# Optimization experiments

Hardware: AMD Instinct MI355X
Metric: run time of the kernel (lower is better)

The kernel has to match this reference:

```python
import jax, jax.numpy as jnp
import numpy as np

B, S, D = 2, 4096, 768
H = 12
HD = D // H  # 64
SCALE = HD ** -0.5


def setup_inputs() -> dict:
    key = jax.random.key(0)
    ks = jax.random.split(key, 5)
    return {
        "x": jax.random.normal(ks[0], (B, S, D), dtype=jnp.float32),
        "qkv_w": jax.random.normal(ks[1], (D, 3 * D), dtype=jnp.float32) * (D ** -0.5),
        "qkv_b": jax.random.normal(ks[2], (3 * D,), dtype=jnp.float32) * 0.02,
        "proj_w": jax.random.normal(ks[3], (D, D), dtype=jnp.float32) * (D ** -0.5),
        "proj_b": jax.random.normal(ks[4], (D,), dtype=jnp.float32) * 0.02,
    }


def reference(x, qkv_w, qkv_b, proj_w, proj_b):
    b, s, d = x.shape
    qkv = x @ qkv_w + qkv_b                      # [B, S, 3D]
    qkv = qkv.reshape(b, s, 3, H, HD)
    q, k, v = jnp.moveaxis(qkv, 2, 0)            # each [B, S, H, HD]
    q = jnp.swapaxes(q, 1, 2)                    # [B, H, S, HD]
    k = jnp.swapaxes(k, 1, 2)
    v = jnp.swapaxes(v, 1, 2)
    attn = jnp.einsum("bhqd,bhkd->bhqk", q, k) * SCALE  # [B, H, S, S]
    attn = jax.nn.softmax(attn, axis=-1)
    out = jnp.einsum("bhqk,bhkd->bhqd", attn, v)        # [B, H, S, HD]
    out = jnp.swapaxes(out, 1, 2).reshape(b, s, d)      # [B, S, D]
    return out @ proj_w + proj_b
```

## Files before the change

### kernel.cpp

```cpp
#include <hip/hip_runtime.h>

typedef unsigned short u16;
typedef __attribute__((ext_vector_type(8))) short bf16x8;
typedef __attribute__((ext_vector_type(4))) float f32x4;
typedef __attribute__((ext_vector_type(16))) float f32x16;

__device__ __forceinline__ u16 f2bf(float f) {
  union { float f; unsigned u; } v; v.f = f;
  unsigned r = v.u + 0x7fffu + ((v.u >> 16) & 1u);
  return (u16)(r >> 16);
}
__device__ __forceinline__ float bf2f(u16 h) {
  union { unsigned u; float f; } v; v.u = ((unsigned)h) << 16;
  return v.f;
}

__device__ __forceinline__ bf16x8 ld_frag(const char* p) {
  union { uint4 u; bf16x8 v; } t;
  t.u = *(const uint4*)p;
  return t.v;
}

__global__ __launch_bounds__(256) void k_prep(const float* __restrict__ x,
                                              const float* __restrict__ qkv_w,
                                              const float* __restrict__ proj_w,
                                              u16* __restrict__ xb,
                                              u16* __restrict__ wt,
                                              u16* __restrict__ pwt) {
  int bid = blockIdx.x, tid = threadIdx.x;
  if (bid < 6144) {
    int i = bid * 256 + tid;
    float4 v = ((const float4*)x)[i];
    ushort4 o; o.x = f2bf(v.x); o.y = f2bf(v.y); o.z = f2bf(v.z); o.w = f2bf(v.w);
    ((ushort4*)xb)[i] = o;
    return;
  }
  __shared__ float tile[32][33];
  const float* in; u16* out; int R, C, bx, by;
  if (bid < 6144 + 1728) {
    int t = bid - 6144; in = qkv_w; out = wt; R = 768; C = 2304;
    bx = (t % 72) * 32; by = (t / 72) * 32;
  } else {
    int t = bid - 7872; in = proj_w; out = pwt; R = 768; C = 768;
    bx = (t % 24) * 32; by = (t / 24) * 32;
  }
  int tx = tid & 31, ty = tid >> 5;
#pragma unroll
  for (int j = 0; j < 32; j += 8)
    tile[ty + j][tx] = in[(size_t)(by + ty + j) * C + bx + tx];
  __syncthreads();
#pragma unroll
  for (int j = 0; j < 32; j += 8)
    out[(size_t)(bx + ty + j) * R + by + tx] = f2bf(tile[tx][ty + j]);
}

#define GAS(p) ((const __attribute__((address_space(1))) void*)(p))
#define LAS(p) ((__attribute__((address_space(3))) void*)(p))

__global__ __launch_bounds__(256) void k_gemm_qkv(
    const u16* __restrict__ A,
    const u16* __restrict__ Bt,
    const float* __restrict__ bias,
    u16* __restrict__ Qb, u16* __restrict__ Kb, u16* __restrict__ Vb) {
  const int K = 768;
  __shared__ u16 Al[128 * 64];
  __shared__ u16 Bl[128 * 64];
  int tn0 = blockIdx.x * 128, tm0 = blockIdx.y * 128;
  int tid = threadIdx.x, w = tid >> 6, lane = tid & 63;
  int l16 = lane & 15, lg = lane >> 4;
  int wm = (w >> 1) * 64, wn = (w & 1) * 64;
  f32x4 acc[4][4];
#pragma unroll
  for (int fm = 0; fm < 4; ++fm)
#pragma unroll
    for (int fn = 0; fn < 4; ++fn) acc[fm][fn] = (f32x4){0.f, 0.f, 0.f, 0.f};
  int srow = w * 32 + (lane >> 3);
  int scol = (lane & 7) * 8;
  for (int k0 = 0; k0 < K; k0 += 64) {
#pragma unroll
    for (int i = 0; i < 4; ++i) {
      __builtin_amdgcn_global_load_lds(GAS(A + (size_t)(tm0 + srow + i * 8) * K + k0 + scol),
                                       LAS((char*)Al + w * 4096 + i * 1024 + lane * 16), 16, 0, 0);
      __builtin_amdgcn_global_load_lds(GAS(Bt + (size_t)(tn0 + srow + i * 8) * K + k0 + scol),
                                       LAS((char*)Bl + w * 4096 + i * 1024 + lane * 16), 16, 0, 0);
    }
    __syncthreads();
#pragma unroll
    for (int ks = 0; ks < 2; ++ks) {
      bf16x8 af[4], bv[4];
#pragma unroll
      for (int f = 0; f < 4; ++f)
        af[f] = *(const bf16x8*)&Al[(wm + f * 16 + l16) * 64 + lg * 8 + ks * 32];
#pragma unroll
      for (int f = 0; f < 4; ++f)
        bv[f] = *(const bf16x8*)&Bl[(wn + f * 16 + l16) * 64 + lg * 8 + ks * 32];
#pragma unroll
      for (int fm = 0; fm < 4; ++fm)
#pragma unroll
        for (int fn = 0; fn < 4; ++fn)
          acc[fm][fn] = __builtin_amdgcn_mfma_f32_16x16x32_bf16(af[fm], bv[fn], acc[fm][fn], 0, 0, 0);
    }
    __syncthreads();
  }
  int part = tn0 / 768;
  u16* dst = part == 0 ? Qb : (part == 1 ? Kb : Vb);
  float qscale = (part == 0) ? 0.18033688011112042f : 1.0f;
#pragma unroll
  for (int fn = 0; fn < 4; ++fn) {
    int nn = tn0 + wn + fn * 16 + l16;
    float bvs = bias[nn];
    int np = nn - part * 768;
    int hh = np >> 6, hd = np & 63;
#pragma unroll
    for (int fm = 0; fm < 4; ++fm) {
#pragma unroll
      for (int r = 0; r < 4; ++r) {
        int m = tm0 + wm + fm * 16 + lg * 4 + r;
        int bb = m >> 12, s = m & 4095;
        size_t idx;
        if (part == 2) {
          int sp = (s & ~12) | ((s & 8) >> 1) | ((s & 4) << 1);
          idx = (((size_t)(bb * 12 + hh)) * 64 + hd) * 4096 + sp;
        } else {
          idx = (((size_t)(bb * 12 + hh)) * 4096 + s) * 64 + hd;
        }
        dst[idx] = f2bf((acc[fm][fn][r] + bvs) * qscale);
      }
    }
  }
}

__global__ __launch_bounds__(256) void k_gemm_proj(
    const u16* __restrict__ A,
    const u16* __restrict__ Bt,
    const float* __restrict__ bias, float* __restrict__ out) {
  const int K = 768;
  __shared__ u16 Al[128 * 64];
  __shared__ u16 Bl[128 * 64];
  int tn0 = blockIdx.x * 128, tm0 = blockIdx.y * 128;
  int tid = threadIdx.x, w = tid >> 6, lane = tid & 63;
  int l16 = lane & 15, lg = lane >> 4;
  int wm = (w >> 1) * 64, wn = (w & 1) * 64;
  f32x4 acc[4][4];
#pragma unroll
  for (int fm = 0; fm < 4; ++fm)
#pragma unroll
    for (int fn = 0; fn < 4; ++fn) acc[fm][fn] = (f32x4){0.f, 0.f, 0.f, 0.f};
  int srow = w * 32 + (lane >> 3);
  int scol = (lane & 7) * 8;
  for (int k0 = 0; k0 < K; k0 += 64) {
#pragma unroll
    for (int i = 0; i < 4; ++i) {
      __builtin_amdgcn_global_load_lds(GAS(A + (size_t)(tm0 + srow + i * 8) * K + k0 + scol),
                                       LAS((char*)Al + w * 4096 + i * 1024 + lane * 16), 16, 0, 0);
      __builtin_amdgcn_global_load_lds(GAS(Bt + (size_t)(tn0 + srow + i * 8) * K + k0 + scol),
                                       LAS((char*)Bl + w * 4096 + i * 1024 + lane * 16), 16, 0, 0);
    }
    __syncthreads();
#pragma unroll
    for (int ks = 0; ks < 2; ++ks) {
      bf16x8 af[4], bv[4];
#pragma unroll
      for (int f = 0; f < 4; ++f)
        af[f] = *(const bf16x8*)&Al[(wm + f * 16 + l16) * 64 + lg * 8 + ks * 32];
#pragma unroll
      for (int f = 0; f < 4; ++f)
        bv[f] = *(const bf16x8*)&Bl[(wn + f * 16 + l16) * 64 + lg * 8 + ks * 32];
#pragma unroll
      for (int fm = 0; fm < 4; ++fm)
#pragma unroll
        for (int fn = 0; fn < 4; ++fn)
          acc[fm][fn] = __builtin_amdgcn_mfma_f32_16x16x32_bf16(af[fm], bv[fn], acc[fm][fn], 0, 0, 0);
    }
    __syncthreads();
  }
#pragma unroll
  for (int fn = 0; fn < 4; ++fn) {
    int nn = tn0 + wn + fn * 16 + l16;
    float bvs = bias[nn];
#pragma unroll
    for (int fm = 0; fm < 4; ++fm) {
#pragma unroll
      for (int r = 0; r < 4; ++r) {
        int m = tm0 + wm + fm * 16 + lg * 4 + r;
        out[(size_t)m * 768 + nn] = acc[fm][fn][r] + bvs;
      }
    }
  }
}

__global__ __launch_bounds__(256, 3) void k_attn(const u16* __restrict__ Qb,
                                                 const u16* __restrict__ Kb,
                                                 const u16* __restrict__ Vtg,
                                                 u16* __restrict__ Ob) {
  const int S = 4096, NH = 12, D = 768;
  __shared__ u16 Kl[2][64 * 64];
  __shared__ u16 Vl[2][64 * 64];

  int bid0 = blockIdx.x;
  int bid = (bid0 & 7) * 96 + (bid0 >> 3);
  int qp = bid & 31;
  int bh = bid >> 5;
  int b = bh / NH, h = bh % NH;
  const u16* Qh = Qb + (size_t)bh * S * 64;
  const char* Khc = (const char*)(Kb + (size_t)bh * S * 64);
  const char* Vhc = (const char*)(Vtg + (size_t)bh * 64 * S);

  int tid = threadIdx.x, w = tid >> 6, lane = tid & 63;
  int q31 = lane & 31, hi = lane >> 5;
  int swb = (q31 & 7) << 4;
  int coff = (hi << 4);

  unsigned xoff[4];
#pragma unroll
  for (int ks = 0; ks < 4; ++ks)
    xoff[ks] = (unsigned)(q31 * 128 + ((ks * 32 + coff) ^ swb));

  int r8 = lane >> 3;
  int chs = (lane & 7) ^ r8;
  const char* kSrc = Khc + (size_t)(w * 16 + r8) * 128 + chs * 16;
  const char* vSrc = Vhc + (size_t)(w * 16 + r8) * 8192 + chs * 16;
  char* kDst0 = (char*)&Kl[0][0] + w * 2048 + lane * 16;
  char* vDst0 = (char*)&Vl[0][0] + w * 2048 + lane * 16;

  auto STAGE = [&](int bufi, int kv) {
#pragma unroll
    for (int qq = 0; qq < 2; ++qq) {
      __builtin_amdgcn_global_load_lds(GAS(kSrc + (size_t)kv * 8192 + qq * 1024),
                                       LAS(kDst0 + bufi * 8192 + qq * 1024), 16, 0, 0);
      __builtin_amdgcn_global_load_lds(GAS(vSrc + (size_t)qq * 65536 + (size_t)kv * 128),
                                       LAS(vDst0 + bufi * 8192 + qq * 1024), 16, 0, 0);
    }
  };

  int qbase = qp * 128 + w * 32;
  const u16* qrow = Qh + (size_t)(qbase + q31) * 64;
  bf16x8 qf[4];
#pragma unroll
  for (int ks = 0; ks < 4; ++ks)
    qf[ks] = *(const bf16x8*)(qrow + ks * 16 + hi * 8);

  f32x16 of0, of1, la0, la1;
#pragma unroll
  for (int i = 0; i < 16; ++i) { of0[i] = 0.f; of1[i] = 0.f; la0[i] = 0.f; la1[i] = 0.f; }

  auto TILE = [&](const char* KB, const char* VB) {
    f32x16 s0, s1;
#pragma unroll
    for (int i = 0; i < 16; ++i) { s0[i] = 0.f; s1[i] = 0.f; }
    __builtin_amdgcn_s_setprio(1);
#pragma unroll
    for (int ks = 0; ks < 4; ++ks) {
      bf16x8 kf = ld_frag(KB + xoff[ks]);
      s0 = __builtin_amdgcn_mfma_f32_32x32x16_bf16(kf, qf[ks], s0, 0, 0, 0);
    }
#pragma unroll
    for (int ks = 0; ks < 4; ++ks) {
      bf16x8 kf = ld_frag(KB + 4096 + xoff[ks]);
      s1 = __builtin_amdgcn_mfma_f32_32x32x16_bf16(kf, qf[ks], s1, 0, 0, 0);
    }
    __builtin_amdgcn_s_setprio(0);
#pragma unroll
    for (int i = 0; i < 16; ++i) {
      s0[i] = __builtin_amdgcn_exp2f(s0[i]);
      s1[i] = __builtin_amdgcn_exp2f(s1[i]);
    }
    la0 += s0;
    la1 += s1;
    union U8 { unsigned u[4]; bf16x8 v; };
    bf16x8 pf[4];
#define MK_PF(DST, SS, R0)                                                        \
    { U8 tt;                                                                      \
      asm("v_cvt_pk_bf16_f32 %0,%1,%2" : "=v"(tt.u[0]) : "v"(SS[R0+0]), "v"(SS[R0+1])); \
      asm("v_cvt_pk_bf16_f32 %0,%1,%2" : "=v"(tt.u[1]) : "v"(SS[R0+2]), "v"(SS[R0+3])); \
      asm("v_cvt_pk_bf16_f32 %0,%1,%2" : "=v"(tt.u[2]) : "v"(SS[R0+4]), "v"(SS[R0+5])); \
      asm("v_cvt_pk_bf16_f32 %0,%1,%2" : "=v"(tt.u[3]) : "v"(SS[R0+6]), "v"(SS[R0+7])); \
      DST = tt.v; }
    MK_PF(pf[0], s0, 0); MK_PF(pf[1], s0, 8);
    MK_PF(pf[2], s1, 0); MK_PF(pf[3], s1, 8);
#undef MK_PF
    __builtin_amdgcn_s_setprio(1);
#pragma unroll
    for (int ks = 0; ks < 4; ++ks) {
      bf16x8 vf = ld_frag(VB + xoff[ks]);
      of0 = __builtin_amdgcn_mfma_f32_32x32x16_bf16(vf, pf[ks], of0, 0, 0, 0);
    }
#pragma unroll
    for (int ks = 0; ks < 4; ++ks) {
      bf16x8 vf = ld_frag(VB + 4096 + xoff[ks]);
      of1 = __builtin_amdgcn_mfma_f32_32x32x16_bf16(vf, pf[ks], of1, 0, 0, 0);
    }
    __builtin_amdgcn_s_setprio(0);
  };

  const char* K0 = (const char*)&Kl[0][0];
  const char* K1 = (const char*)&Kl[1][0];
  const char* V0 = (const char*)&Vl[0][0];
  const char* V1 = (const char*)&Vl[1][0];

  STAGE(0, 0);
  __syncthreads();

#pragma unroll 1
  for (int kv = 0; kv < S / 64; kv += 2) {
    STAGE(1, kv + 1);
    TILE(K0, V0);
    __syncthreads();
    if (kv + 2 < S / 64) STAGE(0, kv + 2);
    TILE(K1, V1);
    if (kv + 2 < S / 64) __syncthreads();
  }

  float ts[8];
#pragma unroll
  for (int i = 0; i < 8; ++i) ts[i] = (la0[i] + la0[i + 8]) + (la1[i] + la1[i + 8]);
#pragma unroll
  for (int st = 4; st >= 1; st >>= 1)
#pragma unroll
    for (int i = 0; i < 4; ++i)
      if (i < st) ts[i] += ts[i + st];
  float l_full = ts[0] + __shfl_xor(ts[0], 32, 64);
  float inv = 1.f / l_full;
  int q = qbase + q31;
  u16* orow = Ob + (size_t)(b * S + q) * D + h * 64;
#pragma unroll
  for (int g = 0; g < 4; ++g) {
    ushort4 o0, o1;
    o0.x = f2bf(of0[g * 4 + 0] * inv); o0.y = f2bf(of0[g * 4 + 1] * inv);
    o0.z = f2bf(of0[g * 4 + 2] * inv); o0.w = f2bf(of0[g * 4 + 3] * inv);
    o1.x = f2bf(of1[g * 4 + 0] * inv); o1.y = f2bf(of1[g * 4 + 1] * inv);
    o1.z = f2bf(of1[g * 4 + 2] * inv); o1.w = f2bf(of1[g * 4 + 3] * inv);
    int hd0 = g * 8 + hi * 4;
    *(ushort4*)(orow + hd0) = o0;
    *(ushort4*)(orow + 32 + hd0) = o1;
  }
}

extern "C" void kernel_launch(void* const* d_in, const int* in_sizes, int n_in,
                              void* d_out, int out_size, void* d_ws, size_t ws_size,
                              hipStream_t stream) {
  const float* x      = (const float*)d_in[0];
  const float* qkv_w  = (const float*)d_in[1];
  const float* qkv_b  = (const float*)d_in[2];
  const float* proj_w = (const float*)d_in[3];
  const float* proj_b = (const float*)d_in[4];
  float* out = (float*)d_out;

  u16* ws  = (u16*)d_ws;
  u16* xb  = ws;
  u16* wt  = xb + 8192 * 768;
  u16* pwt = wt + 2304 * 768;
  u16* Qb  = pwt + 768 * 768;
  u16* Kb  = Qb + 24 * 4096 * 64;
  u16* Vt  = Kb + 24 * 4096 * 64;
  u16* Ob  = Vt + 24 * 4096 * 64;

  k_prep<<<8448, 256, 0, stream>>>(x, qkv_w, proj_w, xb, wt, pwt);
  k_gemm_qkv<<<dim3(18, 64), 256, 0, stream>>>(xb, wt, qkv_b, Qb, Kb, Vt);
  k_attn<<<768, 256, 0, stream>>>(Qb, Kb, Vt, Ob);
  k_gemm_proj<<<dim3(6, 64), 256, 0, stream>>>(Ob, pwt, proj_b, out);
}
```

Baseline: 221.9 us.

## Triple-buffer K/V tiles in attention with partial vmcnt waits

Replaces the double-buffered K/V LDS staging in the attention kernel with a three-stage ring buffer that keeps two tile loads in flight. Barriers now wait only until older loads finish (vmcnt(4)) rather than draining all outstanding loads. The goal is to hide global-to-LDS latency behind MFMA work. LDS use grows from 32KB to 48KB per block, which may limit how many blocks fit per CU under the launch bound of 3.

```diff
diff --git a/kernel.cpp b/kernel.cpp
--- a/kernel.cpp
+++ b/kernel.cpp
@@ -9,10 +9,6 @@
   union { float f; unsigned u; } v; v.f = f;
   unsigned r = v.u + 0x7fffu + ((v.u >> 16) & 1u);
   return (u16)(r >> 16);
-}
-__device__ __forceinline__ float bf2f(u16 h) {
-  union { unsigned u; float f; } v; v.u = ((unsigned)h) << 16;
-  return v.f;
 }
 
 __device__ __forceinline__ bf16x8 ld_frag(const char* p) {
@@ -194,8 +190,7 @@
                                                  const u16* __restrict__ Vtg,
                                                  u16* __restrict__ Ob) {
   const int S = 4096, NH = 12, D = 768;
-  __shared__ u16 Kl[2][64 * 64];
-  __shared__ u16 Vl[2][64 * 64];
+  __shared__ char LDSB[49152];
 
   int bid0 = blockIdx.x;
   int bid = (bid0 & 7) * 96 + (bid0 >> 3);
@@ -220,18 +215,8 @@
   int chs = (lane & 7) ^ r8;
   const char* kSrc = Khc + (size_t)(w * 16 + r8) * 128 + chs * 16;
   const char* vSrc = Vhc + (size_t)(w * 16 + r8) * 8192 + chs * 16;
-  char* kDst0 = (char*)&Kl[0][0] + w * 2048 + lane * 16;
-  char* vDst0 = (char*)&Vl[0][0] + w * 2048 + lane * 16;
-
-  auto STAGE = [&](int bufi, int kv) {
-#pragma unroll
-    for (int qq = 0; qq < 2; ++qq) {
-      __builtin_amdgcn_global_load_lds(GAS(kSrc + (size_t)kv * 8192 + qq * 1024),
-                                       LAS(kDst0 + bufi * 8192 + qq * 1024), 16, 0, 0);
-      __builtin_amdgcn_global_load_lds(GAS(vSrc + (size_t)qq * 65536 + (size_t)kv * 128),
-                                       LAS(vDst0 + bufi * 8192 + qq * 1024), 16, 0, 0);
-    }
-  };
+  char* dstK = LDSB + w * 2048 + lane * 16;
+  char* dstV = dstK + 8192;
 
   int qbase = qp * 128 + w * 32;
   const u16* qrow = Qh + (size_t)(qbase + q31) * 64;
@@ -239,6 +224,23 @@
 #pragma unroll
   for (int ks = 0; ks < 4; ++ks)
     qf[ks] = *(const bf16x8*)(qrow + ks * 16 + hi * 8);
+
+  auto STAGE = [&](int bufi, int kv) {
+#pragma unroll
+    for (int qq = 0; qq < 2; ++qq) {
+      __builtin_amdgcn_global_load_lds(GAS(kSrc + (size_t)kv * 8192 + qq * 1024),
+                                       LAS(dstK + bufi * 16384 + qq * 1024), 16, 0, 0);
+      __builtin_amdgcn_global_load_lds(GAS(vSrc + (size_t)qq * 65536 + (size_t)kv * 128),
+                                       LAS(dstV + bufi * 16384 + qq * 1024), 16, 0, 0);
+    }
+  };
+
+#define BAR4 do { asm volatile("s_waitcnt vmcnt(4)" ::: "memory"); \
+                  __builtin_amdgcn_s_barrier();                    \
+                  asm volatile("" ::: "memory"); } while (0)
+#define BAR0 do { asm volatile("s_waitcnt vmcnt(0)" ::: "memory"); \
+                  __builtin_amdgcn_s_barrier();                    \
+                  asm volatile("" ::: "memory"); } while (0)
 
   f32x16 of0, of1, la0, la1;
 #pragma unroll
@@ -293,23 +295,28 @@
     __builtin_amdgcn_s_setprio(0);
   };
 
-  const char* K0 = (const char*)&Kl[0][0];
-  const char* K1 = (const char*)&Kl[1][0];
-  const char* V0 = (const char*)&Vl[0][0];
-  const char* V1 = (const char*)&Vl[1][0];
+  const char* K0 = LDSB;           const char* V0 = LDSB + 8192;
+  const char* K1 = LDSB + 16384;   const char* V1 = LDSB + 24576;
+  const char* K2 = LDSB + 32768;   const char* V2 = LDSB + 40960;
 
   STAGE(0, 0);
-  __syncthreads();
+  STAGE(1, 1);
+  BAR4;
 
 #pragma unroll 1
-  for (int kv = 0; kv < S / 64; kv += 2) {
-    STAGE(1, kv + 1);
-    TILE(K0, V0);
-    __syncthreads();
-    if (kv + 2 < S / 64) STAGE(0, kv + 2);
-    TILE(K1, V1);
-    if (kv + 2 < S / 64) __syncthreads();
-  }
+  for (int k3 = 0; k3 < 20; ++k3) {
+    int t = k3 * 3;
+    STAGE(2, t + 2); TILE(K0, V0); BAR4;
+    STAGE(0, t + 3); TILE(K1, V1); BAR4;
+    STAGE(1, t + 4); TILE(K2, V2); BAR4;
+  }
+  STAGE(2, 62); TILE(K0, V0); BAR4;
+  STAGE(0, 63); TILE(K1, V1); BAR4;
+  TILE(K2, V2); BAR0;
+  TILE(K0, V0);
+
+#undef BAR4
+#undef BAR0
 
   float ts[8];
 #pragma unroll
```

Measured after the change: 291.6 us. 31.4% more time.
